# Kernel optimization log

Hardware: AMD Instinct MI355X
Metric: run time of the kernel (lower is better)

## Reference

```python
import jax, jax.numpy as jnp
import numpy as np

N_NODES = 100000
N_EDGES = 1000000
N_GRAPHS = 64
IN_F, H_F, N_CLS = 64, 64, 16
N_RELS = 8
N_BASES = 8  # DGL default: num_bases = num_rels when None


def setup_inputs() -> dict:
    key = jax.random.key(0)
    ks = jax.random.split(key, 16)
    in_feat = jax.random.normal(ks[0], (N_NODES, IN_F), dtype=jnp.float32)
    src = jax.random.randint(ks[1], (N_EDGES,), 0, N_NODES)
    dst = jax.random.randint(ks[2], (N_EDGES,), 0, N_NODES)
    etypes = jax.random.randint(ks[3], (N_EDGES,), 0, N_RELS)
    graph_ids = jnp.sort(jax.random.randint(ks[4], (N_NODES,), 0, N_GRAPHS))
    s1 = 1.0 / np.sqrt(IN_F)
    s2 = 1.0 / np.sqrt(H_F)
    bases1 = jax.random.normal(ks[5], (N_BASES, IN_F, H_F), dtype=jnp.float32) * s1
    coeff1 = jax.random.normal(ks[6], (N_RELS, N_BASES), dtype=jnp.float32) * (1.0 / np.sqrt(N_BASES))
    wself1 = jax.random.normal(ks[7], (IN_F, H_F), dtype=jnp.float32) * s1
    bias1 = jnp.zeros((H_F,), dtype=jnp.float32)
    bases2 = jax.random.normal(ks[8], (N_BASES, H_F, N_CLS), dtype=jnp.float32) * s2
    coeff2 = jax.random.normal(ks[9], (N_RELS, N_BASES), dtype=jnp.float32) * (1.0 / np.sqrt(N_BASES))
    wself2 = jax.random.normal(ks[10], (H_F, N_CLS), dtype=jnp.float32) * s2
    bias2 = jnp.zeros((N_CLS,), dtype=jnp.float32)
    return {"in_feat": in_feat, "src": src, "dst": dst, "etypes": etypes,
            "graph_ids": graph_ids, "bases1": bases1, "coeff1": coeff1,
            "wself1": wself1, "bias1": bias1, "bases2": bases2,
            "coeff2": coeff2, "wself2": wself2, "bias2": bias2}


def _rel_graph_conv(x, src, dst, etypes, bases, coeff, wself, bias):
    # Basis decomposition: W_r = sum_b coeff[r,b] * bases[b]
    W = jnp.einsum('rb,bio->rio', coeff, bases)          # [R, in, out]
    # Project every node under every relation (R small), then gather per edge.
    xw = jnp.einsum('ni,rio->rno', x, W)                 # [R, N, out]
    msg = xw[etypes, src]                                 # [E, out]
    agg = jax.ops.segment_sum(msg, dst, num_segments=x.shape[0])
    # DGL defaults: self_loop=True, bias=True
    return agg + x @ wself + bias


def reference(in_feat, src, dst, etypes, graph_ids,
              bases1, coeff1, wself1, bias1,
              bases2, coeff2, wself2, bias2):
    h = _rel_graph_conv(in_feat, src, dst, etypes, bases1, coeff1, wself1, bias1)
    h = jax.nn.relu(h)
    h = _rel_graph_conv(h, src, dst, etypes, bases2, coeff2, wself2, bias2)
    h = jax.nn.relu(h)
    # dgl.mean_nodes: per-graph mean over node features
    sums = jax.ops.segment_sum(h, graph_ids, num_segments=N_GRAPHS)   # [G, C]
    counts = jax.ops.segment_sum(jnp.ones((h.shape[0],), h.dtype), graph_ids,
                                 num_segments=N_GRAPHS)
    return sums / jnp.maximum(counts, 1.0)[:, None]
```

## Files before the change

### kernel.cpp

```cpp
#include <hip/hip_runtime.h>


typedef __attribute__((ext_vector_type(8))) short bf16x8;
typedef __attribute__((ext_vector_type(4))) float f32x4;

#define NBLK1 128

__device__ __forceinline__ unsigned short f2bf(float f) {
    unsigned u = __float_as_uint(f);
    unsigned r = u + 0x7FFFu + ((u >> 16) & 1u);
    return (unsigned short)(r >> 16);
}

__device__ __forceinline__ float bf2f(unsigned short u) {
    return __uint_as_float(((unsigned)u) << 16);
}

__device__ __forceinline__ unsigned pk2(float lo, float hi) {
    unsigned r;
    asm("v_cvt_pk_bf16_f32 %0, %1, %2" : "=v"(r) : "v"(lo), "v"(hi));
    return r;
}

union cv16 { uint4 u; bf16x8 b; };

__global__ __launch_bounds__(256) void k_weights(
    const float* __restrict__ bases1, const float* __restrict__ coeff1,
    const float* __restrict__ bases2, const float* __restrict__ coeff2,
    const float* __restrict__ wself1, const float* __restrict__ wself2,
    unsigned short* __restrict__ W1f, unsigned short* __restrict__ W2f,
    unsigned short* __restrict__ W1sf, unsigned short* __restrict__ W2sf) {
    int r = blockIdx.x;
    int tid = threadIdx.x;
    float c1[8], c2[8];
#pragma unroll
    for (int b = 0; b < 8; ++b) { c1[b] = coeff1[r * 8 + b]; c2[b] = coeff2[r * 8 + b]; }
    for (int idx = tid; idx < 4096; idx += 256) {
        int j = idx & 7, lane = (idx >> 3) & 63, nt = (idx >> 9) & 3, kt = idx >> 11;
        int i = kt * 32 + ((lane >> 4) << 3) + j;
        int jo = nt * 16 + (lane & 15);
        float s = 0.f;
#pragma unroll
        for (int b = 0; b < 8; ++b) s = fmaf(c1[b], bases1[b * 4096 + i * 64 + jo], s);
        W1f[r * 4096 + idx] = f2bf(s);
        if (r == 0) W1sf[idx] = f2bf(wself1[i * 64 + jo]);
    }
    for (int idx = tid; idx < 1024; idx += 256) {
        int j = idx & 7, lane = (idx >> 3) & 63, kt = idx >> 9;
        int i = kt * 32 + ((lane >> 4) << 3) + j;
        int jo = lane & 15;
        float s = 0.f;
#pragma unroll
        for (int b = 0; b < 8; ++b) s = fmaf(c2[b], bases2[b * 1024 + i * 16 + jo], s);
        W2f[r * 1024 + idx] = f2bf(s);
        if (r == 0) W2sf[idx] = f2bf(wself2[i * 16 + jo]);
    }
}

__global__ __launch_bounds__(256) void k_bhist(
    const int* __restrict__ dst, int* __restrict__ bh, int nE, int nBins) {
    __shared__ int h[512];
    for (int i = threadIdx.x; i < 512; i += 256) h[i] = 0;
    __syncthreads();
    int blk = blockIdx.x;
    int ech = (nE + NBLK1 - 1) / NBLK1;
    int e0 = blk * ech, e1 = min(e0 + ech, nE);
    for (int e = e0 + threadIdx.x; e < e1; e += 256)
        atomicAdd(&h[dst[e] >> 8], 1);
    __syncthreads();
    for (int t = threadIdx.x; t < nBins; t += 256) bh[t * NBLK1 + blk] = h[t];
}

__global__ __launch_bounds__(256) void k_scanblk(
    const int* __restrict__ in, int* __restrict__ outx,
    int* __restrict__ btot, int n) {
    __shared__ int sm[256];
    int tid = threadIdx.x;
    int i = blockIdx.x * 256 + tid;
    int d = (i < n) ? in[i] : 0;
    sm[tid] = d;
    __syncthreads();
#pragma unroll
    for (int off = 1; off < 256; off <<= 1) {
        int v = (tid >= off) ? sm[tid - off] : 0;
        __syncthreads();
        sm[tid] += v;
        __syncthreads();
    }
    if (i < n) outx[i] = sm[tid] - d;
    if (tid == 255) btot[blockIdx.x] = sm[255];
}

__global__ void k_scantop(const int* __restrict__ btot, int* __restrict__ boff, int nB) {
    __shared__ int sm[512];
    int t = threadIdx.x;
    int d = (t < nB) ? btot[t] : 0;
    sm[t] = d;
    __syncthreads();
#pragma unroll
    for (int off = 1; off < 512; off <<= 1) {
        int v = (t >= off) ? sm[t - off] : 0;
        __syncthreads();
        sm[t] += v;
        __syncthreads();
    }
    if (t < nB) boff[t] = sm[t] - d;
}

__global__ __launch_bounds__(256) void k_scanadd2(
    int* __restrict__ bhs, const int* __restrict__ boff, int n) {
    int i = blockIdx.x * 256 + threadIdx.x;
    if (i < n) bhs[i] += boff[i >> 8];
}

__global__ __launch_bounds__(256) void k_bscat(
    const int* __restrict__ dst, const int* __restrict__ src,
    const int* __restrict__ et, const int* __restrict__ bhs,
    int* __restrict__ payload, int nE, int nBins) {
    __shared__ int cur[512];
    int blk = blockIdx.x;
    for (int t = threadIdx.x; t < nBins; t += 256) cur[t] = bhs[t * NBLK1 + blk];
    __syncthreads();
    int ech = (nE + NBLK1 - 1) / NBLK1;
    int e0 = blk * ech, e1 = min(e0 + ech, nE);
    for (int e = e0 + threadIdx.x; e < e1; e += 256) {
        int d = dst[e];
        int pos = atomicAdd(&cur[d >> 8], 1);
        payload[pos] = ((src[e] * 8 + et[e]) << 8) | (d & 255);
    }
}

__global__ __launch_bounds__(256) void k_brefine(
    const int* __restrict__ payload, const int* __restrict__ bhs,
    int* __restrict__ skey, int* __restrict__ nodeoff,
    int nE, int nBins, int nNodes) {
    __shared__ int h[256];
    __shared__ int cur[256];
    __shared__ int sm[256];
    int b = blockIdx.x;
    int e0 = bhs[b * NBLK1];
    int e1 = (b + 1 < nBins) ? bhs[(b + 1) * NBLK1] : nE;
    int t = threadIdx.x;
    h[t] = 0;
    __syncthreads();
    for (int e = e0 + t; e < e1; e += 256)
        atomicAdd(&h[payload[e] & 255], 1);
    __syncthreads();
    int d = h[t];
    sm[t] = d;
    __syncthreads();
#pragma unroll
    for (int off = 1; off < 256; off <<= 1) {
        int v = (t >= off) ? sm[t - off] : 0;
        __syncthreads();
        sm[t] += v;
        __syncthreads();
    }
    int excl = sm[t] - d;
    cur[t] = excl;
    int n = (b << 8) + t;
    if (n < nNodes) nodeoff[n] = e0 + excl;
    __syncthreads();
    for (int e = e0 + t; e < e1; e += 256) {
        int pay = payload[e];
        int pos = atomicAdd(&cur[pay & 255], 1);
        skey[e0 + pos] = pay >> 8;
    }
    if (b == 0 && t == 0) nodeoff[nNodes] = nE;
}

#define XW1S 44
__global__ __launch_bounds__(256) void k_xw1(
    const float* __restrict__ x,
    const unsigned short* __restrict__ W1f,
    const unsigned short* __restrict__ W1sf,
    const float* __restrict__ bias1,
    unsigned short* __restrict__ xw1, unsigned short* __restrict__ agg1,
    int nNodes) {
    __shared__ unsigned lds[4][16 * XW1S];
    int lane = threadIdx.x & 63;
    int wid = (int)(threadIdx.x >> 6);
    int tile = blockIdx.x * 4 + wid;
    int n0 = tile * 16;
    if (n0 >= nNodes) return;
    int sA = n0 + (lane & 15);
    if (sA >= nNodes) sA = nNodes - 1;
    const float* xrow = x + (size_t)sA * 64 + ((lane >> 4) << 3);
    bf16x8 a[2];
#pragma unroll
    for (int kt = 0; kt < 2; ++kt) {
        f32x4 u0 = *(const f32x4*)(xrow + kt * 32);
        f32x4 u1 = *(const f32x4*)(xrow + kt * 32 + 4);
        cv16 c;
        c.u.x = pk2(u0[0], u0[1]);
        c.u.y = pk2(u0[2], u0[3]);
        c.u.z = pk2(u1[0], u1[1]);
        c.u.w = pk2(u1[2], u1[3]);
        a[kt] = c.b;
    }
    float bj[4];
#pragma unroll
    for (int nt = 0; nt < 4; ++nt) bj[nt] = bias1[nt * 16 + (lane & 15)];
    unsigned* L = lds[wid];
    const int even = !(lane & 1);
    const int cpair = (lane & 14) >> 1;
    int row2 = lane >> 2, ch = lane & 3;
    int nOut = n0 + row2;
    for (int r = 0; r < 9; ++r) {
        const unsigned short* Wf = (r < 8) ? (W1f + r * 4096) : W1sf;
        f32x4 z = {0.f, 0.f, 0.f, 0.f};
        f32x4 acc[4] = {z, z, z, z};
#pragma unroll
        for (int kt = 0; kt < 2; ++kt)
#pragma unroll
            for (int nt = 0; nt < 4; ++nt) {
                bf16x8 b = *(const bf16x8*)(Wf + (kt * 4 + nt) * 512 + lane * 8);
                acc[nt] = __builtin_amdgcn_mfma_f32_16x16x32_bf16(a[kt], b, acc[nt], 0, 0, 0);
            }
        if (r == 8) {
#pragma unroll
            for (int nt = 0; nt < 4; ++nt)
#pragma unroll
                for (int reg = 0; reg < 4; ++reg) acc[nt][reg] += bj[nt];
        }
#pragma unroll
        for (int reg = 0; reg < 4; ++reg) {
            int row = ((lane >> 4) << 2) + reg;
#pragma unroll
            for (int nt = 0; nt < 4; ++nt) {
                float mine = acc[nt][reg];
                float oth = __shfl_xor(mine, 1, 64);
                unsigned pk = even ? pk2(mine, oth) : pk2(oth, mine);
                if (even ? (nt < 2) : (nt >= 2)) L[row * XW1S + cpair + nt * 8] = pk;
            }
        }
        if (nOut < nNodes) {
            uint4 v0 = *(uint4*)&L[row2 * XW1S + ch * 4];
            uint4 v1 = *(uint4*)&L[row2 * XW1S + 16 + ch * 4];
            uint4* mp = (r < 8) ? (uint4*)(xw1 + ((size_t)nOut * 8 + r) * 64)
                                : (uint4*)(agg1 + (size_t)nOut * 64);
            mp[ch] = v0;
            mp[4 + ch] = v1;
        }
    }
}

__device__ __forceinline__ void acc8(uint4 m, float* a) {
    a[0] += bf2f((unsigned short)m.x); a[1] += bf2f((unsigned short)(m.x >> 16));
    a[2] += bf2f((unsigned short)m.y); a[3] += bf2f((unsigned short)(m.y >> 16));
    a[4] += bf2f((unsigned short)m.z); a[5] += bf2f((unsigned short)(m.z >> 16));
    a[6] += bf2f((unsigned short)m.w); a[7] += bf2f((unsigned short)(m.w >> 16));
}

__global__ __launch_bounds__(256) void k_seg1f(
    const unsigned short* __restrict__ xw1, const int* __restrict__ skey,
    const int* __restrict__ nodeoff, unsigned short* __restrict__ agg1,
    int nNodes) {
    int gl = threadIdx.x & 7;
    int grp = (int)((blockIdx.x * blockDim.x + threadIdx.x) >> 3);
    int nG = (int)((gridDim.x * blockDim.x) >> 3);
    for (int n = grp; n < nNodes; n += nG) {
        int s0 = nodeoff[n], s1 = nodeoff[n + 1];
        uint4 v = *(const uint4*)(agg1 + (size_t)n * 64 + gl * 8);
        float a[8];
        a[0] = bf2f((unsigned short)v.x); a[1] = bf2f((unsigned short)(v.x >> 16));
        a[2] = bf2f((unsigned short)v.y); a[3] = bf2f((unsigned short)(v.y >> 16));
        a[4] = bf2f((unsigned short)v.z); a[5] = bf2f((unsigned short)(v.z >> 16));
        a[6] = bf2f((unsigned short)v.w); a[7] = bf2f((unsigned short)(v.w >> 16));
        int i = s0;
        for (; i + 4 <= s1; i += 4) {
            int k0 = skey[i], k1 = skey[i + 1], k2 = skey[i + 2], k3 = skey[i + 3];
            uint4 m0 = *(const uint4*)(xw1 + (size_t)k0 * 64 + gl * 8);
            uint4 m1 = *(const uint4*)(xw1 + (size_t)k1 * 64 + gl * 8);
            uint4 m2 = *(const uint4*)(xw1 + (size_t)k2 * 64 + gl * 8);
            uint4 m3 = *(const uint4*)(xw1 + (size_t)k3 * 64 + gl * 8);
            acc8(m0, a); acc8(m1, a); acc8(m2, a); acc8(m3, a);
        }
        for (; i < s1; ++i) {
            int key = skey[i];
            uint4 m = *(const uint4*)(xw1 + (size_t)key * 64 + gl * 8);
            acc8(m, a);
        }
#pragma unroll
        for (int q = 0; q < 8; ++q) a[q] = fmaxf(a[q], 0.f);
        uint4 p;
        p.x = pk2(a[0], a[1]);
        p.y = pk2(a[2], a[3]);
        p.z = pk2(a[4], a[5]);
        p.w = pk2(a[6], a[7]);
        *(uint4*)(agg1 + (size_t)n * 64 + gl * 8) = p;
    }
}

__global__ __launch_bounds__(256) void k_xw2(
    const unsigned short* __restrict__ h,
    const unsigned short* __restrict__ W2f,
    const unsigned short* __restrict__ W2sf,
    const float* __restrict__ bias2,
    unsigned short* __restrict__ xw2, unsigned short* __restrict__ agg2,
    int nNodes) {
    __shared__ unsigned lds[4][16 * 12];
    int lane = threadIdx.x & 63;
    int wid = (int)(threadIdx.x >> 6);
    int tile = blockIdx.x * 4 + wid;
    int n0 = tile * 16;
    if (n0 >= nNodes) return;
    int sA = n0 + (lane & 15);
    if (sA >= nNodes) sA = nNodes - 1;
    const unsigned short* hrow = h + (size_t)sA * 64 + ((lane >> 4) << 3);
    bf16x8 a[2];
    a[0] = *(const bf16x8*)(hrow);
    a[1] = *(const bf16x8*)(hrow + 32);
    float bj = bias2[lane & 15];
    unsigned* L = lds[wid];
    const int even = !(lane & 1);
    const int cpair = (lane & 14) >> 1;
    int row2 = lane >> 1, ch = lane & 1;
    int nOut = n0 + row2;
    for (int r = 0; r < 9; ++r) {
        const unsigned short* Wf = (r < 8) ? (W2f + r * 1024) : W2sf;
        bf16x8 b0 = *(const bf16x8*)(Wf + lane * 8);
        bf16x8 b1 = *(const bf16x8*)(Wf + 512 + lane * 8);
        f32x4 acc = {0.f, 0.f, 0.f, 0.f};
        acc = __builtin_amdgcn_mfma_f32_16x16x32_bf16(a[0], b0, acc, 0, 0, 0);
        acc = __builtin_amdgcn_mfma_f32_16x16x32_bf16(a[1], b1, acc, 0, 0, 0);
        if (r == 8) {
#pragma unroll
            for (int reg = 0; reg < 4; ++reg) acc[reg] += bj;
        }
#pragma unroll
        for (int reg = 0; reg < 4; ++reg) {
            int row = ((lane >> 4) << 2) + reg;
            float mine = acc[reg];
            float oth = __shfl_xor(mine, 1, 64);
            unsigned pk = even ? pk2(mine, oth) : pk2(oth, mine);
            if (even ? (reg < 2) : (reg >= 2)) L[row * 12 + cpair] = pk;
        }
        if (lane < 32 && nOut < nNodes) {
            uint4 v = *(uint4*)&L[row2 * 12 + ch * 4];
            uint4* mp = (r < 8) ? (uint4*)(xw2 + ((size_t)nOut * 8 + r) * 16)
                                : (uint4*)(agg2 + (size_t)nOut * 16);
            mp[ch] = v;
        }
    }
}

__global__ __launch_bounds__(256) void k_seg2f(
    const unsigned short* __restrict__ xw2, const int* __restrict__ skey,
    const int* __restrict__ nodeoff, unsigned short* __restrict__ agg2,
    int nNodes) {
    int gl = threadIdx.x & 1;
    int grp = (int)((blockIdx.x * blockDim.x + threadIdx.x) >> 1);
    int nG = (int)((gridDim.x * blockDim.x) >> 1);
    for (int n = grp; n < nNodes; n += nG) {
        int s0 = nodeoff[n], s1 = nodeoff[n + 1];
        uint4 v = *(const uint4*)(agg2 + (size_t)n * 16 + gl * 8);
        float a[8];
        a[0] = bf2f((unsigned short)v.x); a[1] = bf2f((unsigned short)(v.x >> 16));
        a[2] = bf2f((unsigned short)v.y); a[3] = bf2f((unsigned short)(v.y >> 16));
        a[4] = bf2f((unsigned short)v.z); a[5] = bf2f((unsigned short)(v.z >> 16));
        a[6] = bf2f((unsigned short)v.w); a[7] = bf2f((unsigned short)(v.w >> 16));
        int i = s0;
        for (; i + 4 <= s1; i += 4) {
            int k0 = skey[i], k1 = skey[i + 1], k2 = skey[i + 2], k3 = skey[i + 3];
            uint4 m0 = *(const uint4*)(xw2 + (size_t)k0 * 16 + gl * 8);
            uint4 m1 = *(const uint4*)(xw2 + (size_t)k1 * 16 + gl * 8);
            uint4 m2 = *(const uint4*)(xw2 + (size_t)k2 * 16 + gl * 8);
            uint4 m3 = *(const uint4*)(xw2 + (size_t)k3 * 16 + gl * 8);
            acc8(m0, a); acc8(m1, a); acc8(m2, a); acc8(m3, a);
        }
        for (; i < s1; ++i) {
            int key = skey[i];
            uint4 m = *(const uint4*)(xw2 + (size_t)key * 16 + gl * 8);
            acc8(m, a);
        }
        uint4 p;
        p.x = pk2(a[0], a[1]);
        p.y = pk2(a[2], a[3]);
        p.z = pk2(a[4], a[5]);
        p.w = pk2(a[6], a[7]);
        *(uint4*)(agg2 + (size_t)n * 16 + gl * 8) = p;
    }
}

__global__ __launch_bounds__(256) void k_pool(
    const unsigned short* __restrict__ agg2, const int* __restrict__ gid,
    float* __restrict__ out, int nNodes) {
    __shared__ float sm[256];
    __shared__ int bnd[2];
    int g = blockIdx.x;
    int t = threadIdx.x;
    if (t < 2) {
        int target = g + t;
        int lo = 0, hi = nNodes;
        while (lo < hi) {
            int mid = (lo + hi) >> 1;
            if (gid[mid] < target) lo = mid + 1; else hi = mid;
        }
        bnd[t] = lo;
    }
    __syncthreads();
    int s0 = bnd[0], s1 = bnd[1];
    int c = t & 15, idx = t >> 4;
    float acc = 0.f;
    for (int n = s0 + idx; n < s1; n += 16) acc += fmaxf(bf2f(agg2[(size_t)n * 16 + c]), 0.f);
    sm[t] = acc;
    __syncthreads();
#pragma unroll
    for (int off = 128; off >= 16; off >>= 1) {
        if (t < off) sm[t] += sm[t + off];
        __syncthreads();
    }
    if (t < 16) {
        float cnt = (float)(s1 - s0);
        out[g * 16 + t] = sm[t] / fmaxf(cnt, 1.f);
    }
}

extern "C" void kernel_launch(void* const* d_in, const int* in_sizes, int n_in,
                              void* d_out, int out_size, void* d_ws, size_t ws_size,
                              hipStream_t stream) {
    const float* x      = (const float*)d_in[0];
    const int*   src    = (const int*)d_in[1];
    const int*   dst    = (const int*)d_in[2];
    const int*   et     = (const int*)d_in[3];
    const int*   gid    = (const int*)d_in[4];
    const float* bases1 = (const float*)d_in[5];
    const float* coeff1 = (const float*)d_in[6];
    const float* wself1 = (const float*)d_in[7];
    const float* bias1  = (const float*)d_in[8];
    const float* bases2 = (const float*)d_in[9];
    const float* coeff2 = (const float*)d_in[10];
    const float* wself2 = (const float*)d_in[11];
    const float* bias2  = (const float*)d_in[12];
    float* out = (float*)d_out;

    int nNodes = in_sizes[0] / 64;
    int nE = in_sizes[1];
    int nBins = (nNodes + 255) >> 8;
    int nBh = nBins * NBLK1;

    char* ws = (char*)d_ws;
    unsigned short* W1f  = (unsigned short*)(ws);
    unsigned short* W2f  = (unsigned short*)(ws + 65536);
    unsigned short* W1sf = (unsigned short*)(ws + 81920);
    unsigned short* W2sf = (unsigned short*)(ws + 90112);
    unsigned short* agg1 = (unsigned short*)(ws + 12892160);
    unsigned short* agg2 = (unsigned short*)(ws + 25692160);
    int*   payload = (int*)(ws + 28892160);
    int*   skey    = (int*)(ws + 32892160);
    int*   nodeoff = (int*)(ws + 36892160);
    int*   bh      = (int*)(ws + 37292224);
    int*   bhs     = (int*)(ws + 37492416);
    int*   btot    = (int*)(ws + 37692608);
    int*   boff    = (int*)(ws + 37694656);
    unsigned short* xw1 = (unsigned short*)(ws + 37697024);
    unsigned short* xw2 = xw1;

    int tiles = (nNodes + 15) / 16;
    int xwb = (tiles + 3) / 4;
    int scb = (nBh + 255) / 256;

    hipLaunchKernelGGL(k_weights, dim3(8), dim3(256), 0, stream,
                       bases1, coeff1, bases2, coeff2, wself1, wself2,
                       W1f, W2f, W1sf, W2sf);
    hipLaunchKernelGGL(k_bhist, dim3(NBLK1), dim3(256), 0, stream,
                       dst, bh, nE, nBins);
    hipLaunchKernelGGL(k_scanblk, dim3(scb), dim3(256), 0, stream,
                       bh, bhs, btot, nBh);
    hipLaunchKernelGGL(k_scantop, dim3(1), dim3(512), 0, stream, btot, boff, scb);
    hipLaunchKernelGGL(k_scanadd2, dim3(scb), dim3(256), 0, stream,
                       bhs, boff, nBh);
    hipLaunchKernelGGL(k_bscat, dim3(NBLK1), dim3(256), 0, stream,
                       dst, src, et, bhs, payload, nE, nBins);
    hipLaunchKernelGGL(k_brefine, dim3(nBins), dim3(256), 0, stream,
                       payload, bhs, skey, nodeoff, nE, nBins, nNodes);
    hipLaunchKernelGGL(k_xw1, dim3(xwb), dim3(256), 0, stream,
                       x, W1f, W1sf, bias1, xw1, agg1, nNodes);
    hipLaunchKernelGGL(k_seg1f, dim3(2048), dim3(256), 0, stream,
                       xw1, skey, nodeoff, agg1, nNodes);
    hipLaunchKernelGGL(k_xw2, dim3(xwb), dim3(256), 0, stream,
                       agg1, W2f, W2sf, bias2, xw2, agg2, nNodes);
    hipLaunchKernelGGL(k_seg2f, dim3(1024), dim3(256), 0, stream,
                       xw2, skey, nodeoff, agg2, nNodes);
    hipLaunchKernelGGL(k_pool, dim3(64), dim3(256), 0, stream,
                       agg2, gid, out, nNodes);
}
```

Measured before the change: 193.9 us.

## Fuse layer-1 aggregation with layer-2 projection and collapse the scan kernels

Merges the weight-combination kernel into the histogram kernel as extra blocks, replaces the three-kernel multi-block scan with a single 1024-thread scan, and doubles the histogram/scatter block count. The layer-1 gather-sum now writes relu'd rows into shared memory and immediately runs the layer-2 MFMA projection, removing the agg1 round trip through global memory and one launch. Node projections switch to an interleaved layout of 9 rows per node (8 relations plus self), so edge keys become src*9+et and self-loop values sit next to the relation rows. In exchange, the fused kernel uses smaller fixed 64-node blocks with a block-wide sync, and the single-block scan serialises that step.

```diff
diff --git a/kernel.cpp b/kernel.cpp
--- a/kernel.cpp
+++ b/kernel.cpp
@@ -4,7 +4,7 @@
 typedef __attribute__((ext_vector_type(8))) short bf16x8;
 typedef __attribute__((ext_vector_type(4))) float f32x4;
 
-#define NBLK1 128
+#define NBLK 256
 
 __device__ __forceinline__ unsigned short f2bf(float f) {
     unsigned u = __float_as_uint(f);
@@ -24,93 +24,79 @@
 
 union cv16 { uint4 u; bf16x8 b; };
 
-__global__ __launch_bounds__(256) void k_weights(
+__device__ __forceinline__ void acc8(uint4 m, float* a) {
+    a[0] += bf2f((unsigned short)m.x); a[1] += bf2f((unsigned short)(m.x >> 16));
+    a[2] += bf2f((unsigned short)m.y); a[3] += bf2f((unsigned short)(m.y >> 16));
+    a[4] += bf2f((unsigned short)m.z); a[5] += bf2f((unsigned short)(m.z >> 16));
+    a[6] += bf2f((unsigned short)m.w); a[7] += bf2f((unsigned short)(m.w >> 16));
+}
+
+__global__ __launch_bounds__(256) void k_bhist_w(
+    const int* __restrict__ dst, int* __restrict__ bh, int nE, int nBins,
     const float* __restrict__ bases1, const float* __restrict__ coeff1,
     const float* __restrict__ bases2, const float* __restrict__ coeff2,
     const float* __restrict__ wself1, const float* __restrict__ wself2,
     unsigned short* __restrict__ W1f, unsigned short* __restrict__ W2f,
     unsigned short* __restrict__ W1sf, unsigned short* __restrict__ W2sf) {
-    int r = blockIdx.x;
-    int tid = threadIdx.x;
-    float c1[8], c2[8];
-#pragma unroll
-    for (int b = 0; b < 8; ++b) { c1[b] = coeff1[r * 8 + b]; c2[b] = coeff2[r * 8 + b]; }
-    for (int idx = tid; idx < 4096; idx += 256) {
-        int j = idx & 7, lane = (idx >> 3) & 63, nt = (idx >> 9) & 3, kt = idx >> 11;
-        int i = kt * 32 + ((lane >> 4) << 3) + j;
-        int jo = nt * 16 + (lane & 15);
-        float s = 0.f;
-#pragma unroll
-        for (int b = 0; b < 8; ++b) s = fmaf(c1[b], bases1[b * 4096 + i * 64 + jo], s);
-        W1f[r * 4096 + idx] = f2bf(s);
-        if (r == 0) W1sf[idx] = f2bf(wself1[i * 64 + jo]);
-    }
-    for (int idx = tid; idx < 1024; idx += 256) {
-        int j = idx & 7, lane = (idx >> 3) & 63, kt = idx >> 9;
-        int i = kt * 32 + ((lane >> 4) << 3) + j;
-        int jo = lane & 15;
-        float s = 0.f;
-#pragma unroll
-        for (int b = 0; b < 8; ++b) s = fmaf(c2[b], bases2[b * 1024 + i * 16 + jo], s);
-        W2f[r * 1024 + idx] = f2bf(s);
-        if (r == 0) W2sf[idx] = f2bf(wself2[i * 16 + jo]);
-    }
-}
-
-__global__ __launch_bounds__(256) void k_bhist(
-    const int* __restrict__ dst, int* __restrict__ bh, int nE, int nBins) {
+    if (blockIdx.x >= NBLK) {
+        int r = blockIdx.x - NBLK;
+        int tid = threadIdx.x;
+        float c1[8], c2[8];
+#pragma unroll
+        for (int b = 0; b < 8; ++b) { c1[b] = coeff1[r * 8 + b]; c2[b] = coeff2[r * 8 + b]; }
+        for (int idx = tid; idx < 4096; idx += 256) {
+            int j = idx & 7, lane = (idx >> 3) & 63, nt = (idx >> 9) & 3, kt = idx >> 11;
+            int i = kt * 32 + ((lane >> 4) << 3) + j;
+            int jo = nt * 16 + (lane & 15);
+            float s = 0.f;
+#pragma unroll
+            for (int b = 0; b < 8; ++b) s = fmaf(c1[b], bases1[b * 4096 + i * 64 + jo], s);
+            W1f[r * 4096 + idx] = f2bf(s);
+            if (r == 0) W1sf[idx] = f2bf(wself1[i * 64 + jo]);
+        }
+        for (int idx = tid; idx < 1024; idx += 256) {
+            int j = idx & 7, lane = (idx >> 3) & 63, kt = idx >> 9;
+            int i = kt * 32 + ((lane >> 4) << 3) + j;
+            int jo = lane & 15;
+            float s = 0.f;
+#pragma unroll
+            for (int b = 0; b < 8; ++b) s = fmaf(c2[b], bases2[b * 1024 + i * 16 + jo], s);
+            W2f[r * 1024 + idx] = f2bf(s);
+            if (r == 0) W2sf[idx] = f2bf(wself2[i * 16 + jo]);
+        }
+        return;
+    }
     __shared__ int h[512];
     for (int i = threadIdx.x; i < 512; i += 256) h[i] = 0;
     __syncthreads();
     int blk = blockIdx.x;
-    int ech = (nE + NBLK1 - 1) / NBLK1;
+    int ech = (nE + NBLK - 1) / NBLK;
     int e0 = blk * ech, e1 = min(e0 + ech, nE);
     for (int e = e0 + threadIdx.x; e < e1; e += 256)
         atomicAdd(&h[dst[e] >> 8], 1);
     __syncthreads();
-    for (int t = threadIdx.x; t < nBins; t += 256) bh[t * NBLK1 + blk] = h[t];
-}
-
-__global__ __launch_bounds__(256) void k_scanblk(
-    const int* __restrict__ in, int* __restrict__ outx,
-    int* __restrict__ btot, int n) {
-    __shared__ int sm[256];
-    int tid = threadIdx.x;
-    int i = blockIdx.x * 256 + tid;
-    int d = (i < n) ? in[i] : 0;
-    sm[tid] = d;
-    __syncthreads();
-#pragma unroll
-    for (int off = 1; off < 256; off <<= 1) {
-        int v = (tid >= off) ? sm[tid - off] : 0;
+    for (int t = threadIdx.x; t < nBins; t += 256) bh[t * NBLK + blk] = h[t];
+}
+
+__global__ __launch_bounds__(1024) void k_scan(
+    const int* __restrict__ bh, int* __restrict__ bhs, int n) {
+    __shared__ int tot[1024];
+    int t = threadIdx.x;
+    int S = (n + 1023) / 1024;
+    int i0 = t * S, i1 = min(i0 + S, n);
+    int s = 0;
+    for (int i = i0; i < i1; ++i) s += bh[i];
+    tot[t] = s;
+    __syncthreads();
+#pragma unroll
+    for (int off = 1; off < 1024; off <<= 1) {
+        int v = (t >= off) ? tot[t - off] : 0;
         __syncthreads();
-        sm[tid] += v;
+        tot[t] += v;
         __syncthreads();
     }
-    if (i < n) outx[i] = sm[tid] - d;
-    if (tid == 255) btot[blockIdx.x] = sm[255];
-}
-
-__global__ void k_scantop(const int* __restrict__ btot, int* __restrict__ boff, int nB) {
-    __shared__ int sm[512];
-    int t = threadIdx.x;
-    int d = (t < nB) ? btot[t] : 0;
-    sm[t] = d;
-    __syncthreads();
-#pragma unroll
-    for (int off = 1; off < 512; off <<= 1) {
-        int v = (t >= off) ? sm[t - off] : 0;
-        __syncthreads();
-        sm[t] += v;
-        __syncthreads();
-    }
-    if (t < nB) boff[t] = sm[t] - d;
-}
-
-__global__ __launch_bounds__(256) void k_scanadd2(
-    int* __restrict__ bhs, const int* __restrict__ boff, int n) {
-    int i = blockIdx.x * 256 + threadIdx.x;
-    if (i < n) bhs[i] += boff[i >> 8];
+    int run = tot[t] - s;
+    for (int i = i0; i < i1; ++i) { int d = bh[i]; bhs[i] = run; run += d; }
 }
 
 __global__ __launch_bounds__(256) void k_bscat(
@@ -119,14 +105,14 @@
     int* __restrict__ payload, int nE, int nBins) {
     __shared__ int cur[512];
     int blk = blockIdx.x;
-    for (int t = threadIdx.x; t < nBins; t += 256) cur[t] = bhs[t * NBLK1 + blk];
-    __syncthreads();
-    int ech = (nE + NBLK1 - 1) / NBLK1;
+    for (int t = threadIdx.x; t < nBins; t += 256) cur[t] = bhs[t * NBLK + blk];
+    __syncthreads();
+    int ech = (nE + NBLK - 1) / NBLK;
     int e0 = blk * ech, e1 = min(e0 + ech, nE);
     for (int e = e0 + threadIdx.x; e < e1; e += 256) {
         int d = dst[e];
         int pos = atomicAdd(&cur[d >> 8], 1);
-        payload[pos] = ((src[e] * 8 + et[e]) << 8) | (d & 255);
+        payload[pos] = ((src[e] * 9 + et[e]) << 8) | (d & 255);
     }
 }
 
@@ -138,8 +124,8 @@
     __shared__ int cur[256];
     __shared__ int sm[256];
     int b = blockIdx.x;
-    int e0 = bhs[b * NBLK1];
-    int e1 = (b + 1 < nBins) ? bhs[(b + 1) * NBLK1] : nE;
+    int e0 = bhs[b * NBLK];
+    int e1 = (b + 1 < nBins) ? bhs[(b + 1) * NBLK] : nE;
     int t = threadIdx.x;
     h[t] = 0;
     __syncthreads();
@@ -175,8 +161,7 @@
     const unsigned short* __restrict__ W1f,
     const unsigned short* __restrict__ W1sf,
     const float* __restrict__ bias1,
-    unsigned short* __restrict__ xw1, unsigned short* __restrict__ agg1,
-    int nNodes) {
+    unsigned short* __restrict__ xw1, int nNodes) {
     __shared__ unsigned lds[4][16 * XW1S];
     int lane = threadIdx.x & 63;
     int wid = (int)(threadIdx.x >> 6);
@@ -237,93 +222,81 @@
         if (nOut < nNodes) {
             uint4 v0 = *(uint4*)&L[row2 * XW1S + ch * 4];
             uint4 v1 = *(uint4*)&L[row2 * XW1S + 16 + ch * 4];
-            uint4* mp = (r < 8) ? (uint4*)(xw1 + ((size_t)nOut * 8 + r) * 64)
-                                : (uint4*)(agg1 + (size_t)nOut * 64);
+            uint4* mp = (uint4*)(xw1 + ((size_t)nOut * 9 + r) * 64);
             mp[ch] = v0;
             mp[4 + ch] = v1;
         }
     }
 }
 
-__device__ __forceinline__ void acc8(uint4 m, float* a) {
-    a[0] += bf2f((unsigned short)m.x); a[1] += bf2f((unsigned short)(m.x >> 16));
-    a[2] += bf2f((unsigned short)m.y); a[3] += bf2f((unsigned short)(m.y >> 16));
-    a[4] += bf2f((unsigned short)m.z); a[5] += bf2f((unsigned short)(m.z >> 16));
-    a[6] += bf2f((unsigned short)m.w); a[7] += bf2f((unsigned short)(m.w >> 16));
-}
-
-__global__ __launch_bounds__(256) void k_seg1f(
+__global__ __launch_bounds__(256) void k_f1(
     const unsigned short* __restrict__ xw1, const int* __restrict__ skey,
-    const int* __restrict__ nodeoff, unsigned short* __restrict__ agg1,
-    int nNodes) {
-    int gl = threadIdx.x & 7;
-    int grp = (int)((blockIdx.x * blockDim.x + threadIdx.x) >> 3);
-    int nG = (int)((gridDim.x * blockDim.x) >> 3);
-    for (int n = grp; n < nNodes; n += nG) {
-        int s0 = nodeoff[n], s1 = nodeoff[n + 1];
-        uint4 v = *(const uint4*)(agg1 + (size_t)n * 64 + gl * 8);
-        float a[8];
-        a[0] = bf2f((unsigned short)v.x); a[1] = bf2f((unsigned short)(v.x >> 16));
-        a[2] = bf2f((unsigned short)v.y); a[3] = bf2f((unsigned short)(v.y >> 16));
-        a[4] = bf2f((unsigned short)v.z); a[5] = bf2f((unsigned short)(v.z >> 16));
-        a[6] = bf2f((unsigned short)v.w); a[7] = bf2f((unsigned short)(v.w >> 16));
-        int i = s0;
-        for (; i + 4 <= s1; i += 4) {
-            int k0 = skey[i], k1 = skey[i + 1], k2 = skey[i + 2], k3 = skey[i + 3];
-            uint4 m0 = *(const uint4*)(xw1 + (size_t)k0 * 64 + gl * 8);
-            uint4 m1 = *(const uint4*)(xw1 + (size_t)k1 * 64 + gl * 8);
-            uint4 m2 = *(const uint4*)(xw1 + (size_t)k2 * 64 + gl * 8);
-            uint4 m3 = *(const uint4*)(xw1 + (size_t)k3 * 64 + gl * 8);
-            acc8(m0, a); acc8(m1, a); acc8(m2, a); acc8(m3, a);
-        }
-        for (; i < s1; ++i) {
-            int key = skey[i];
-            uint4 m = *(const uint4*)(xw1 + (size_t)key * 64 + gl * 8);
-            acc8(m, a);
-        }
-#pragma unroll
-        for (int q = 0; q < 8; ++q) a[q] = fmaxf(a[q], 0.f);
-        uint4 p;
-        p.x = pk2(a[0], a[1]);
-        p.y = pk2(a[2], a[3]);
-        p.z = pk2(a[4], a[5]);
-        p.w = pk2(a[6], a[7]);
-        *(uint4*)(agg1 + (size_t)n * 64 + gl * 8) = p;
-    }
-}
-
-__global__ __launch_bounds__(256) void k_xw2(
-    const unsigned short* __restrict__ h,
+    const int* __restrict__ nodeoff,
     const unsigned short* __restrict__ W2f,
     const unsigned short* __restrict__ W2sf,
     const float* __restrict__ bias2,
-    unsigned short* __restrict__ xw2, unsigned short* __restrict__ agg2,
-    int nNodes) {
-    __shared__ unsigned lds[4][16 * 12];
-    int lane = threadIdx.x & 63;
-    int wid = (int)(threadIdx.x >> 6);
-    int tile = blockIdx.x * 4 + wid;
-    int n0 = tile * 16;
-    if (n0 >= nNodes) return;
-    int sA = n0 + (lane & 15);
-    if (sA >= nNodes) sA = nNodes - 1;
-    const unsigned short* hrow = h + (size_t)sA * 64 + ((lane >> 4) << 3);
-    bf16x8 a[2];
-    a[0] = *(const bf16x8*)(hrow);
-    a[1] = *(const bf16x8*)(hrow + 32);
+    unsigned short* __restrict__ xw2, int nNodes) {
+    __shared__ uint4 hbuf[64][9];
+    __shared__ unsigned tlds[4][16 * 12];
+    int t = threadIdx.x;
+    int n0blk = blockIdx.x * 64;
+    int gl = t & 7;
+    int grp = t >> 3;
+    for (int pass = 0; pass < 2; ++pass) {
+        int nn = pass * 32 + grp;
+        int n = n0blk + nn;
+        uint4 p = {0, 0, 0, 0};
+        if (n < nNodes) {
+            int s0 = nodeoff[n], s1 = nodeoff[n + 1];
+            uint4 v = *(const uint4*)(xw1 + ((size_t)n * 9 + 8) * 64 + gl * 8);
+            float a[8];
+            a[0] = bf2f((unsigned short)v.x); a[1] = bf2f((unsigned short)(v.x >> 16));
+            a[2] = bf2f((unsigned short)v.y); a[3] = bf2f((unsigned short)(v.y >> 16));
+            a[4] = bf2f((unsigned short)v.z); a[5] = bf2f((unsigned short)(v.z >> 16));
+            a[6] = bf2f((unsigned short)v.w); a[7] = bf2f((unsigned short)(v.w >> 16));
+            int i = s0;
+            for (; i + 4 <= s1; i += 4) {
+                int k0 = skey[i], k1 = skey[i + 1], k2 = skey[i + 2], k3 = skey[i + 3];
+                uint4 m0 = *(const uint4*)(xw1 + (size_t)k0 * 64 + gl * 8);
+                uint4 m1 = *(const uint4*)(xw1 + (size_t)k1 * 64 + gl * 8);
+                uint4 m2 = *(const uint4*)(xw1 + (size_t)k2 * 64 + gl * 8);
+                uint4 m3 = *(const uint4*)(xw1 + (size_t)k3 * 64 + gl * 8);
+                acc8(m0, a); acc8(m1, a); acc8(m2, a); acc8(m3, a);
+            }
+            for (; i < s1; ++i) {
+                uint4 m = *(const uint4*)(xw1 + (size_t)skey[i] * 64 + gl * 8);
+                acc8(m, a);
+            }
+#pragma unroll
+            for (int q = 0; q < 8; ++q) a[q] = fmaxf(a[q], 0.f);
+            p.x = pk2(a[0], a[1]);
+            p.y = pk2(a[2], a[3]);
+            p.z = pk2(a[4], a[5]);
+            p.w = pk2(a[6], a[7]);
+        }
+        hbuf[nn][gl] = p;
+    }
+    __syncthreads();
+    int lane = t & 63;
+    int w = t >> 6;
+    int arow = w * 16 + (lane & 15);
+    cv16 c0, c1;
+    c0.u = hbuf[arow][lane >> 4];
+    c1.u = hbuf[arow][4 + (lane >> 4)];
+    bf16x8 a0 = c0.b, a1 = c1.b;
     float bj = bias2[lane & 15];
-    unsigned* L = lds[wid];
+    unsigned* L = tlds[w];
     const int even = !(lane & 1);
     const int cpair = (lane & 14) >> 1;
     int row2 = lane >> 1, ch = lane & 1;
-    int nOut = n0 + row2;
+    int nOut = n0blk + w * 16 + row2;
     for (int r = 0; r < 9; ++r) {
         const unsigned short* Wf = (r < 8) ? (W2f + r * 1024) : W2sf;
         bf16x8 b0 = *(const bf16x8*)(Wf + lane * 8);
         bf16x8 b1 = *(const bf16x8*)(Wf + 512 + lane * 8);
         f32x4 acc = {0.f, 0.f, 0.f, 0.f};
-        acc = __builtin_amdgcn_mfma_f32_16x16x32_bf16(a[0], b0, acc, 0, 0, 0);
-        acc = __builtin_amdgcn_mfma_f32_16x16x32_bf16(a[1], b1, acc, 0, 0, 0);
+        acc = __builtin_amdgcn_mfma_f32_16x16x32_bf16(a0, b0, acc, 0, 0, 0);
+        acc = __builtin_amdgcn_mfma_f32_16x16x32_bf16(a1, b1, acc, 0, 0, 0);
         if (r == 8) {
 #pragma unroll
             for (int reg = 0; reg < 4; ++reg) acc[reg] += bj;
@@ -338,23 +311,20 @@
         }
         if (lane < 32 && nOut < nNodes) {
             uint4 v = *(uint4*)&L[row2 * 12 + ch * 4];
-            uint4* mp = (r < 8) ? (uint4*)(xw2 + ((size_t)nOut * 8 + r) * 16)
-                                : (uint4*)(agg2 + (size_t)nOut * 16);
-            mp[ch] = v;
+            ((uint4*)(xw2 + ((size_t)nOut * 9 + r) * 16))[ch] = v;
         }
     }
 }
 
 __global__ __launch_bounds__(256) void k_seg2f(
-    const unsigned short* __restrict__ xw2, const int* __restrict__ skey,
-    const int* __restrict__ nodeoff, unsigned short* __restrict__ agg2,
-    int nNodes) {
+    unsigned short* __restrict__ xw2, const int* __restrict__ skey,
+    const int* __restrict__ nodeoff, int nNodes) {
     int gl = threadIdx.x & 1;
     int grp = (int)((blockIdx.x * blockDim.x + threadIdx.x) >> 1);
     int nG = (int)((gridDim.x * blockDim.x) >> 1);
     for (int n = grp; n < nNodes; n += nG) {
         int s0 = nodeoff[n], s1 = nodeoff[n + 1];
-        uint4 v = *(const uint4*)(agg2 + (size_t)n * 16 + gl * 8);
+        uint4 v = *(const uint4*)(xw2 + ((size_t)n * 9 + 8) * 16 + gl * 8);
         float a[8];
         a[0] = bf2f((unsigned short)v.x); a[1] = bf2f((unsigned short)(v.x >> 16));
         a[2] = bf2f((unsigned short)v.y); a[3] = bf2f((unsigned short)(v.y >> 16));
@@ -370,8 +340,7 @@
             acc8(m0, a); acc8(m1, a); acc8(m2, a); acc8(m3, a);
         }
         for (; i < s1; ++i) {
-            int key = skey[i];
-            uint4 m = *(const uint4*)(xw2 + (size_t)key * 16 + gl * 8);
+            uint4 m = *(const uint4*)(xw2 + (size_t)skey[i] * 16 + gl * 8);
             acc8(m, a);
         }
         uint4 p;
@@ -379,12 +348,12 @@
         p.y = pk2(a[2], a[3]);
         p.z = pk2(a[4], a[5]);
         p.w = pk2(a[6], a[7]);
-        *(uint4*)(agg2 + (size_t)n * 16 + gl * 8) = p;
+        *(uint4*)(xw2 + ((size_t)n * 9 + 8) * 16 + gl * 8) = p;
     }
 }
 
 __global__ __launch_bounds__(256) void k_pool(
-    const unsigned short* __restrict__ agg2, const int* __restrict__ gid,
+    const unsigned short* __restrict__ xw2, const int* __restrict__ gid,
     float* __restrict__ out, int nNodes) {
     __shared__ float sm[256];
     __shared__ int bnd[2];
@@ -403,7 +372,8 @@
     int s0 = bnd[0], s1 = bnd[1];
     int c = t & 15, idx = t >> 4;
     float acc = 0.f;
-    for (int n = s0 + idx; n < s1; n += 16) acc += fmaxf(bf2f(agg2[(size_t)n * 16 + c]), 0.f);
+    for (int n = s0 + idx; n < s1; n += 16)
+        acc += fmaxf(bf2f(xw2[((size_t)n * 9 + 8) * 16 + c]), 0.f);
     sm[t] = acc;
     __syncthreads();
 #pragma unroll
@@ -438,51 +408,40 @@
     int nNodes = in_sizes[0] / 64;
     int nE = in_sizes[1];
     int nBins = (nNodes + 255) >> 8;
-    int nBh = nBins * NBLK1;
+    int nBh = nBins * NBLK;
 
     char* ws = (char*)d_ws;
     unsigned short* W1f  = (unsigned short*)(ws);
     unsigned short* W2f  = (unsigned short*)(ws + 65536);
     unsigned short* W1sf = (unsigned short*)(ws + 81920);
     unsigned short* W2sf = (unsigned short*)(ws + 90112);
-    unsigned short* agg1 = (unsigned short*)(ws + 12892160);
-    unsigned short* agg2 = (unsigned short*)(ws + 25692160);
-    int*   payload = (int*)(ws + 28892160);
-    int*   skey    = (int*)(ws + 32892160);
-    int*   nodeoff = (int*)(ws + 36892160);
-    int*   bh      = (int*)(ws + 37292224);
-    int*   bhs     = (int*)(ws + 37492416);
-    int*   btot    = (int*)(ws + 37692608);
-    int*   boff    = (int*)(ws + 37694656);
-    unsigned short* xw1 = (unsigned short*)(ws + 37697024);
-    unsigned short* xw2 = xw1;
+    int*   payload = (int*)(ws + 92160);
+    int*   skey    = (int*)(ws + 4092160);
+    int*   nodeoff = (int*)(ws + 8092160);
+    int*   bh      = (int*)(ws + 8492288);
+    int*   bhs     = (int*)(ws + 8892672);
+    unsigned short* xw1 = (unsigned short*)(ws + 9293056);
+    unsigned short* xw2 = (unsigned short*)(ws + 124493056);
 
     int tiles = (nNodes + 15) / 16;
     int xwb = (tiles + 3) / 4;
-    int scb = (nBh + 255) / 256;
-
-    hipLaunchKernelGGL(k_weights, dim3(8), dim3(256), 0, stream,
+    int f1b = (nNodes + 63) / 64;
+
+    hipLaunchKernelGGL(k_bhist_w, dim3(NBLK + 8), dim3(256), 0, stream,
+                       dst, bh, nE, nBins,
                        bases1, coeff1, bases2, coeff2, wself1, wself2,
                        W1f, W2f, W1sf, W2sf);
-    hipLaunchKernelGGL(k_bhist, dim3(NBLK1), dim3(256), 0, stream,
-                       dst, bh, nE, nBins);
-    hipLaunchKernelGGL(k_scanblk, dim3(scb), dim3(256), 0, stream,
-                       bh, bhs, btot, nBh);
-    hipLaunchKernelGGL(k_scantop, dim3(1), dim3(512), 0, stream, btot, boff, scb);
-    hipLaunchKernelGGL(k_scanadd2, dim3(scb), dim3(256), 0, stream,
-                       bhs, boff, nBh);
-    hipLaunchKernelGGL(k_bscat, dim3(NBLK1), dim3(256), 0, stream,
+    hipLaunchKernelGGL(k_scan, dim3(1), dim3(1024), 0, stream, bh, bhs, nBh);
+    hipLaunchKernelGGL(k_bscat, dim3(NBLK), dim3(256), 0, stream,
                        dst, src, et, bhs, payload, nE, nBins);
     hipLaunchKernelGGL(k_brefine, dim3(nBins), dim3(256), 0, stream,
                        payload, bhs, skey, nodeoff, nE, nBins, nNodes);
     hipLaunchKernelGGL(k_xw1, dim3(xwb), dim3(256), 0, stream,
-                       x, W1f, W1sf, bias1, xw1, agg1, nNodes);
-    hipLaunchKernelGGL(k_seg1f, dim3(2048), dim3(256), 0, stream,
-                       xw1, skey, nodeoff, agg1, nNodes);
-    hipLaunchKernelGGL(k_xw2, dim3(xwb), dim3(256), 0, stream,
-                       agg1, W2f, W2sf, bias2, xw2, agg2, nNodes);
+                       x, W1f, W1sf, bias1, xw1, nNodes);
+    hipLaunchKernelGGL(k_f1, dim3(f1b), dim3(256), 0, stream,
+                       xw1, skey, nodeoff, W2f, W2sf, bias2, xw2, nNodes);
     hipLaunchKernelGGL(k_seg2f, dim3(1024), dim3(256), 0, stream,
-                       xw2, skey, nodeoff, agg2, nNodes);
+                       xw2, skey, nodeoff, nNodes);
     hipLaunchKernelGGL(k_pool, dim3(64), dim3(256), 0, stream,
-                       agg2, gid, out, nNodes);
-}
+                       xw2, gid, out, nNodes);
+}
```

Result: slower. 328.1 us (+69.2%).
